# Kernel optimization log

Hardware: AMD Instinct MI355X
Metric: run time of the kernel (lower is better)

Reference implementation:

```python
import jax, jax.numpy as jnp
import numpy as np

# dims
B = 16        # batch
S = 32        # question seq len
H = 768       # bert-base hidden
E = 200000    # num entities
T = 200000    # padded triples per example
R = 500       # num relations
STEPS = 3     # num_steps
WAYS = 2      # num_ways


def setup_inputs() -> dict:
    key = jax.random.key(0)
    ks = jax.random.split(key, 10)
    # one-hot head entity per example (start distribution)
    head_ids = jax.random.randint(ks[0], (B,), 0, E)
    heads = jnp.zeros((B, E), jnp.float32).at[jnp.arange(B), head_ids].set(1.0)
    q_embeddings = jax.random.normal(ks[1], (B, H), jnp.float32)
    q_word_h = jax.random.normal(ks[2], (B, S, H), jnp.float32)
    attention_mask = jnp.ones((B, S), jnp.float32)
    # padded per-example triples (sub, rel, obj)
    sub = jax.random.randint(ks[3], (B, T), 0, E)
    rel = jax.random.randint(ks[4], (B, T), 0, R)
    obj = jax.random.randint(ks[5], (B, T), 0, E)
    triples = jnp.stack([sub, rel, obj], axis=-1).astype(jnp.int32)  # [B,T,3]
    scale = 0.02
    step_W = jax.random.normal(ks[6], (WAYS, STEPS, H, H), jnp.float32) * scale
    step_b = jnp.zeros((WAYS, STEPS, H), jnp.float32)
    rel_W = jax.random.normal(ks[7], (WAYS, H, R), jnp.float32) * scale
    rel_b = jnp.zeros((WAYS, R), jnp.float32)
    hop_W = jax.random.normal(ks[8], (WAYS, H, STEPS), jnp.float32) * scale
    hop_b = jnp.zeros((WAYS, STEPS), jnp.float32)
    return dict(heads=heads, q_embeddings=q_embeddings, q_word_h=q_word_h,
                attention_mask=attention_mask, step_W=step_W, step_b=step_b,
                rel_W=rel_W, rel_b=rel_b, hop_W=hop_W, hop_b=hop_b,
                triples=triples)


def _propagate(last_e, triples, rel_dist):
    # last_e: [E], triples: [T,3], rel_dist: [R] -> [E]
    sub, rel, obj = triples[:, 0], triples[:, 1], triples[:, 2]
    obj_p = last_e[sub] * rel_dist[rel]                 # gather + gate  [T]
    return jax.ops.segment_sum(obj_p, obj, num_segments=E)  # scatter-add [E]


def reference(heads, q_embeddings, q_word_h, attention_mask,
              step_W, step_b, rel_W, rel_b, hop_W, hop_b, triples):
    e_score = []
    for w in range(WAYS):
        last_e = heads                                   # [B,E]
        ent_probs = []
        for t in range(STEPS):
            cq_t = jnp.tanh(q_embeddings @ step_W[w, t] + step_b[w, t])   # [B,H]
            q_logits = jnp.einsum('bh,bsh->bs', cq_t, q_word_h)            # [B,S]
            q_dist = jax.nn.softmax(q_logits, axis=1) * attention_mask
            q_dist = q_dist / (jnp.sum(q_dist, axis=1, keepdims=True) + 1e-6)
            ctx_h = jnp.einsum('bs,bsh->bh', q_dist, q_word_h)             # [B,H]
            rel_dist = jax.nn.sigmoid(ctx_h @ rel_W[w] + rel_b[w])         # [B,R]
            last_e = jax.vmap(_propagate)(last_e, triples, rel_dist)      # [B,E]
            # renormalize entries > 1 (detached divisor, as in original)
            z = jax.lax.stop_gradient(jnp.where(last_e > 1.0, last_e, 1.0))
            last_e = last_e / z
            ent_probs.append(last_e)
        hop_res = jnp.stack(ent_probs, axis=1)                             # [B,STEPS,E]
        hop_attn = jax.nn.softmax(q_embeddings @ hop_W[w] + hop_b[w], axis=1)  # [B,STEPS]
        e_score.append(jnp.einsum('bse,bs->be', hop_res, hop_attn))
    return jnp.prod(jnp.stack(e_score), axis=0)                            # [B,E]
```

## Files before the change

kernel.cpp:

```cpp
#include <hip/hip_runtime.h>
#include <math.h>

#define NB 16
#define NS 32
#define NH 768
#define NE 200000
#define NT 200000
#define NR 500
#define NSTEPS 3
#define NWAYS 2

#define HSZ 2048
#define AHSZ 4096
#define BMW 6272
#define PCHUNK 40

typedef unsigned int u32;

__device__ __forceinline__ int fhash(int e) { return (int)(((u32)e * 2654435761u) >> 21); }
__device__ __forceinline__ int ahash(int e) { return (int)(((u32)e * 2654435761u) >> 20); }

__global__ __launch_bounds__(256) void cq_part_kernel(
    const float* __restrict__ qe, const float* __restrict__ stepW,
    float* __restrict__ part)
{
    int blk = blockIdx.x;
    int jc = blk % 12;
    int wt = (blk / 12) % 6;
    int kc = blk / 72;

    __shared__ float s_w[192][68];
    __shared__ float s_q[NB][196];

    int tid = threadIdx.x;
    int lane = tid & 63, wv = tid >> 6;

    {
        const float* Wbase = stepW + (size_t)wt * NH * NH + (size_t)(kc * 192) * NH + jc * 64;
#pragma unroll
        for (int u = 0; u < 12; ++u) {
            int f = tid + u * 256;
            int hh = f >> 4, c4 = (f & 15) * 4;
            float4 v = *(const float4*)(Wbase + (size_t)hh * NH + c4);
            *(float4*)&s_w[hh][c4] = v;
        }
    }
    {
#pragma unroll
        for (int u = 0; u < 3; ++u) {
            int f = tid + u * 256;
            int b = f / 48, c4 = (f % 48) * 4;
            float4 v = *(const float4*)(qe + (size_t)b * NH + kc * 192 + c4);
            *(float4*)&s_q[b][c4] = v;
        }
    }
    __syncthreads();

    float acc[4] = {0.f, 0.f, 0.f, 0.f};
#pragma unroll 4
    for (int h4 = 0; h4 < 48; ++h4) {
        float w0 = s_w[h4 * 4 + 0][lane];
        float w1 = s_w[h4 * 4 + 1][lane];
        float w2 = s_w[h4 * 4 + 2][lane];
        float w3 = s_w[h4 * 4 + 3][lane];
#pragma unroll
        for (int i = 0; i < 4; ++i) {
            float4 q = *(const float4*)&s_q[wv * 4 + i][h4 * 4];
            acc[i] += w0 * q.x + w1 * q.y + w2 * q.z + w3 * q.w;
        }
    }
#pragma unroll
    for (int i = 0; i < 4; ++i) {
        int b = wv * 4 + i;
        part[(((size_t)kc * 6 + wt) * NB + b) * NH + jc * 64 + lane] = acc[i];
    }
}

__global__ __launch_bounds__(256) void attn_kernel(
    const float* __restrict__ part, const float* __restrict__ stepB,
    const float* __restrict__ qwh, const float* __restrict__ mask,
    float* __restrict__ ctx)
{
    int b = blockIdx.x % NB;
    int wt = blockIdx.x / NB;

    __shared__ float s_cq[NH];
    __shared__ float s_sm[NS];

    int tid = threadIdx.x;

    for (int j = tid; j < NH; j += 256) {
        float a = stepB[wt * NH + j];
#pragma unroll
        for (int kc = 0; kc < 4; ++kc)
            a += part[(((size_t)kc * 6 + wt) * NB + b) * NH + j];
        s_cq[j] = tanhf(a);
    }
    __syncthreads();

    {
        int s = tid >> 3, l = tid & 7;
        const float* row = qwh + ((size_t)b * NS + s) * NH;
        float a = 0.f;
        for (int h = l; h < NH; h += 8) a += s_cq[h] * row[h];
        a += __shfl_down(a, 4, 8);
        a += __shfl_down(a, 2, 8);
        a += __shfl_down(a, 1, 8);
        if (l == 0) s_sm[s] = a;
    }
    __syncthreads();

    if (tid < 64) {
        float lg = (tid < 32) ? s_sm[tid] : -1e30f;
        float m = lg;
        for (int off = 16; off; off >>= 1) m = fmaxf(m, __shfl_xor(m, off, 32));
        float ev = expf(lg - m);
        float sum = ev;
        for (int off = 16; off; off >>= 1) sum += __shfl_xor(sum, off, 32);
        float d = ev / sum * ((tid < 32) ? mask[b * NS + tid] : 0.f);
        float sum2 = d;
        for (int off = 16; off; off >>= 1) sum2 += __shfl_xor(sum2, off, 32);
        d = d / (sum2 + 1e-6f);
        if (tid < 32) s_sm[tid] = d;
    }
    __syncthreads();

    for (int h = tid; h < NH; h += 256) {
        const float* col = qwh + (size_t)b * NS * NH + h;
        float c = 0.f;
#pragma unroll 8
        for (int s = 0; s < NS; ++s) c += s_sm[s] * col[s * NH];
        ctx[((size_t)wt * NB + b) * NH + h] = c;
    }
}

__global__ __launch_bounds__(256) void rel_part_kernel(
    const float* __restrict__ ctx, const float* __restrict__ relW,
    float* __restrict__ part_r)
{
    int blk = blockIdx.x;
    int rc = blk & 7;
    int w  = (blk >> 3) & 1;
    int kc = blk >> 4;

    __shared__ float s_ctx[48][68];

    int tid = threadIdx.x;
    int lane = tid & 63, wv = tid >> 6;

#pragma unroll
    for (int u = 0; u < 3; ++u) {
        int f = tid + u * 256;
        int tb = f >> 4, c4 = (f & 15) * 4;
        int t = tb >> 4, b = tb & 15;
        float4 v = *(const float4*)(ctx + ((size_t)(w * 3 + t) * NB + b) * NH + kc * 64 + c4);
        *(float4*)&s_ctx[tb][c4] = v;
    }
    __syncthreads();

    int col = rc * 64 + lane;
    int colc = col < NR ? col : NR - 1;
    const float* Wb = relW + (size_t)w * NH * NR + (size_t)(kc * 64) * NR + colc;

    float acc[12];
#pragma unroll
    for (int i = 0; i < 12; ++i) acc[i] = 0.f;

#pragma unroll 4
    for (int h4 = 0; h4 < 16; ++h4) {
        float w0 = Wb[(size_t)(h4 * 4 + 0) * NR];
        float w1 = Wb[(size_t)(h4 * 4 + 1) * NR];
        float w2 = Wb[(size_t)(h4 * 4 + 2) * NR];
        float w3 = Wb[(size_t)(h4 * 4 + 3) * NR];
#pragma unroll
        for (int i = 0; i < 12; ++i) {
            float4 c = *(const float4*)&s_ctx[wv * 12 + i][h4 * 4];
            acc[i] += w0 * c.x + w1 * c.y + w2 * c.z + w3 * c.w;
        }
    }
    if (col < NR) {
#pragma unroll
        for (int i = 0; i < 12; ++i) {
            int tb = wv * 12 + i;
            int t = tb >> 4, b = tb & 15;
            part_r[(((size_t)kc * 6 + (w * 3 + t)) * NB + b) * NR + col] = acc[i];
        }
    }
}

__global__ void rel_reduce_kernel(const float* __restrict__ part_r,
                                  const float* __restrict__ relB,
                                  float* __restrict__ rel)
{
    int b = blockIdx.x % NB;
    int wt = blockIdx.x / NB;
    int w = wt / NSTEPS;
    for (int r = threadIdx.x; r < NR; r += 256) {
        float a = relB[w * NR + r];
#pragma unroll
        for (int kc = 0; kc < 12; ++kc)
            a += part_r[(((size_t)kc * 6 + wt) * NB + b) * NR + r];
        rel[((size_t)wt * NB + b) * NR + r] = 1.f / (1.f + expf(-a));
    }
}

__global__ __launch_bounds__(192) void hop_kernel(
    const float* __restrict__ qe, const float* __restrict__ hopW,
    const float* __restrict__ hopB, float* __restrict__ hop)
{
    int wb = blockIdx.x;
    int w = wb / NB, b = wb % NB;
    int t = threadIdx.x / 64, l = threadIdx.x % 64;
    __shared__ float s_logit[4];
    float a = 0.f;
    for (int h = l; h < NH; h += 64) a += qe[b * NH + h] * hopW[((size_t)w * NH + h) * NSTEPS + t];
    for (int off = 32; off; off >>= 1) a += __shfl_down(a, off, 64);
    if (l == 0) s_logit[t] = a + hopB[w * NSTEPS + t];
    __syncthreads();
    if (threadIdx.x == 0) {
        float mx = fmaxf(s_logit[0], fmaxf(s_logit[1], s_logit[2]));
        float e0 = expf(s_logit[0] - mx), e1 = expf(s_logit[1] - mx), e2 = expf(s_logit[2] - mx);
        float inv = 1.f / (e0 + e1 + e2);
        hop[wb * NSTEPS + 0] = e0 * inv;
        hop[wb * NSTEPS + 1] = e1 * inv;
        hop[wb * NSTEPS + 2] = e2 * inv;
    }
}

__global__ void head_kernel(const float* __restrict__ heads, int* __restrict__ keys0,
                            float* __restrict__ vals0, u32* __restrict__ bm0)
{
    size_t N4 = (size_t)NB * NE / 4;
    const float4* h4 = (const float4*)heads;
    for (size_t i = (size_t)blockIdx.x * blockDim.x + threadIdx.x; i < N4;
         i += (size_t)gridDim.x * blockDim.x) {
        float4 v = h4[i];
        float c[4] = { v.x, v.y, v.z, v.w };
#pragma unroll
        for (int k = 0; k < 4; ++k) {
            if (c[k] != 0.0f) {
                size_t idx = i * 4 + k;
                int b = (int)(idx / NE);
                int e = (int)(idx % NE);
                int s = fhash(e);
                keys0[(size_t)b * HSZ + s] = e + 1;
                vals0[(size_t)b * HSZ + s] = 1.0f;
                vals0[(size_t)(NB + b) * HSZ + s] = 1.0f;
                atomicOr(&bm0[(size_t)b * BMW + (e >> 5)], 1u << (e & 31));
            }
        }
    }
}

__global__ __launch_bounds__(256) void prop_kernel(
    const int* __restrict__ triples,
    const u32* __restrict__ bmIn, const int* __restrict__ keysIn, const float* __restrict__ valsIn,
    u32* __restrict__ bmOut, int* __restrict__ keysOut, float* __restrict__ valsOut,
    const float* __restrict__ rel, int t)
{
    __shared__ u32 s_bm[BMW];
    int b = blockIdx.x / PCHUNK;
    int c = blockIdx.x % PCHUNK;
    const u32* g = bmIn + (size_t)b * BMW;
    for (int k = threadIdx.x; k < BMW; k += 256) s_bm[k] = g[k];
    __syncthreads();

    const int*   kin  = keysIn  + (size_t)b * HSZ;
    const float* v0in = valsIn  + (size_t)b * HSZ;
    const float* v1in = valsIn  + (size_t)(NB + b) * HSZ;
    const float* r0 = rel + ((size_t)(0 * NSTEPS + t) * NB + b) * NR;
    const float* r1 = rel + ((size_t)(1 * NSTEPS + t) * NB + b) * NR;
    int*   kout  = keysOut + (size_t)b * HSZ;
    float* v0out = valsOut + (size_t)b * HSZ;
    float* v1out = valsOut + (size_t)(NB + b) * HSZ;
    u32*   bmo   = bmOut + (size_t)b * BMW;

    const int4* tp = (const int4*)(triples + (size_t)b * NT * 3);
    const int QPC = (NT / 4) / PCHUNK;
    int qend = (c + 1) * QPC;
    for (int q = c * QPC + threadIdx.x; q < qend; q += 256) {
        int4 x = tp[q * 3 + 0];
        int4 y = tp[q * 3 + 1];
        int4 z = tp[q * 3 + 2];
        int su[4] = { x.x, x.w, y.z, z.y };
        int re[4] = { x.y, y.x, y.w, z.z };
        int ob[4] = { x.z, y.y, z.x, z.w };
#pragma unroll
        for (int k = 0; k < 4; ++k) {
            int sub = su[k];
            if ((s_bm[sub >> 5] >> (sub & 31)) & 1u) {
                int s = fhash(sub);
                float v0 = 0.f, v1 = 0.f;
                bool found = false;
                for (int p = 0; p < HSZ; ++p) {
                    int kk = kin[s];
                    if (kk == 0) break;
                    if (kk == sub + 1) {
                        v0 = fminf(v0in[s], 1.0f);
                        v1 = fminf(v1in[s], 1.0f);
                        found = true;
                        break;
                    }
                    s = (s + 1) & (HSZ - 1);
                }
                if (found) {
                    float c0 = v0 * r0[re[k]];
                    float c1 = v1 * r1[re[k]];
                    int e = ob[k];
                    int s2 = fhash(e);
                    for (int p = 0; p < HSZ; ++p) {
                        int old = atomicCAS(&kout[s2], 0, e + 1);
                        if (old == 0 || old == e + 1) {
                            atomicAdd(&v0out[s2], c0);
                            atomicAdd(&v1out[s2], c1);
                            if (old == 0) atomicOr(&bmo[e >> 5], 1u << (e & 31));
                            break;
                        }
                        s2 = (s2 + 1) & (HSZ - 1);
                    }
                }
            }
        }
    }
}

__global__ __launch_bounds__(256) void final_kernel(
    const int* __restrict__ keysG, const float* __restrict__ valsG,
    const float* __restrict__ hop, float* __restrict__ out)
{
    __shared__ int s_k[AHSZ];
    __shared__ float s_v0[AHSZ];
    __shared__ float s_v1[AHSZ];
    int b = blockIdx.x;
    for (int i = threadIdx.x; i < AHSZ; i += 256) { s_k[i] = 0; s_v0[i] = 0.f; s_v1[i] = 0.f; }
    __syncthreads();
    for (int gen = 1; gen <= 3; ++gen) {
        const int* kg = keysG + ((size_t)gen * NB + b) * HSZ;
        const float* vg = valsG + (size_t)gen * NWAYS * NB * HSZ;
        const float* v0 = vg + (size_t)b * HSZ;
        const float* v1 = vg + (size_t)(NB + b) * HSZ;
        float h0 = hop[(0 * NB + b) * NSTEPS + (gen - 1)];
        float h1 = hop[(1 * NB + b) * NSTEPS + (gen - 1)];
        for (int i = threadIdx.x; i < HSZ; i += 256) {
            int key = kg[i];
            if (key == 0) continue;
            float a0 = h0 * fminf(v0[i], 1.0f);
            float a1 = h1 * fminf(v1[i], 1.0f);
            int s = ahash(key - 1);
            for (int p = 0; p < AHSZ; ++p) {
                int old = atomicCAS(&s_k[s], 0, key);
                if (old == 0 || old == key) {
                    atomicAdd(&s_v0[s], a0);
                    atomicAdd(&s_v1[s], a1);
                    break;
                }
                s = (s + 1) & (AHSZ - 1);
            }
        }
    }
    __syncthreads();
    for (int i = threadIdx.x; i < AHSZ; i += 256) {
        int key = s_k[i];
        if (key) out[(size_t)b * NE + (key - 1)] = s_v0[i] * s_v1[i];
    }
}

extern "C" void kernel_launch(void* const* d_in, const int* in_sizes, int n_in,
                              void* d_out, int out_size, void* d_ws, size_t ws_size,
                              hipStream_t stream)
{
    const float* heads  = (const float*)d_in[0];
    const float* qe     = (const float*)d_in[1];
    const float* qwh    = (const float*)d_in[2];
    const float* mask   = (const float*)d_in[3];
    const float* stepW  = (const float*)d_in[4];
    const float* stepB  = (const float*)d_in[5];
    const float* relW   = (const float*)d_in[6];
    const float* relB   = (const float*)d_in[7];
    const float* hopW   = (const float*)d_in[8];
    const float* hopB   = (const float*)d_in[9];
    const int*   triples = (const int*)d_in[10];
    float* out = (float*)d_out;

    int*   keysG = (int*)d_ws;
    float* valsG = (float*)(keysG + 4 * NB * HSZ);
    u32*   bmG   = (u32*)(valsG + 4 * NWAYS * NB * HSZ);
    float* rel   = (float*)(bmG + 4 * (size_t)NB * BMW);
    float* hop   = rel + (size_t)NWAYS * NSTEPS * NB * NR;
    float* part  = hop + NWAYS * NB * NSTEPS;
    float* ctx   = part + (size_t)4 * 6 * NB * NH;
    float* part_r = ctx + (size_t)6 * NB * NH;

    size_t zero_bytes = (char*)rel - (char*)d_ws;
    hipMemsetAsync(d_ws, 0, zero_bytes, stream);
    hipMemsetAsync(d_out, 0, (size_t)NB * NE * sizeof(float), stream);

    cq_part_kernel<<<288, 256, 0, stream>>>(qe, stepW, part);
    hop_kernel<<<NWAYS * NB, 192, 0, stream>>>(qe, hopW, hopB, hop);
    head_kernel<<<2048, 256, 0, stream>>>(heads, keysG, valsG, bmG);
    attn_kernel<<<96, 256, 0, stream>>>(part, stepB, qwh, mask, ctx);
    rel_part_kernel<<<192, 256, 0, stream>>>(ctx, relW, part_r);
    rel_reduce_kernel<<<96, 256, 0, stream>>>(part_r, relB, rel);

    for (int t = 0; t < NSTEPS; ++t) {
        prop_kernel<<<NB * PCHUNK, 256, 0, stream>>>(
            triples,
            bmG + (size_t)t * NB * BMW,
            keysG + (size_t)t * NB * HSZ,
            valsG + (size_t)t * NWAYS * NB * HSZ,
            bmG + (size_t)(t + 1) * NB * BMW,
            keysG + (size_t)(t + 1) * NB * HSZ,
            valsG + (size_t)(t + 1) * NWAYS * NB * HSZ,
            rel, t);
    }

    final_kernel<<<NB, 256, 0, stream>>>(keysG, valsG, hop, out);
}
```

Measured before the change: 211.4 us.

## Fuse whole pipeline into one cooperative persistent kernel with grid syncs

Replaces the memsets and roughly ten separate kernel launches with a single cooperative kernel of 256 blocks. Phases are separated by grid.sync: zeroing, cq with fused tanh, head/hop, attention, the rel matmul, three propagation steps, and the final combine. The cq K-split reduction is folded into each block, and the rel sigmoid is computed on demand from partial sums. The aim is to remove launch overhead and inter-kernel gaps. The cost is fewer blocks for the propagation phase, redundant rel recomputation, and grid-wide barrier latency; a multi-launch fallback is kept in case the cooperative launch fails.

```diff
diff --git a/kernel.cpp b/kernel.cpp
--- a/kernel.cpp
+++ b/kernel.cpp
@@ -1,5 +1,8 @@
 #include <hip/hip_runtime.h>
+#include <hip/hip_cooperative_groups.h>
 #include <math.h>
+
+namespace cg = cooperative_groups;
 
 #define NB 16
 #define NS 32
@@ -13,355 +16,330 @@
 #define HSZ 2048
 #define AHSZ 4096
 #define BMW 6272
-#define PCHUNK 40
+#define GRID 256
+#define PCH 16
+#define QPB 50000
+#define QPC 3125
 
 typedef unsigned int u32;
 
 __device__ __forceinline__ int fhash(int e) { return (int)(((u32)e * 2654435761u) >> 21); }
 __device__ __forceinline__ int ahash(int e) { return (int)(((u32)e * 2654435761u) >> 20); }
 
-__global__ __launch_bounds__(256) void cq_part_kernel(
-    const float* __restrict__ qe, const float* __restrict__ stepW,
-    float* __restrict__ part)
+union SharedU {
+    struct { float w[192][68]; float q[NB][196]; } cq;
+    struct { u32 bm[BMW]; } pr;
+    struct { float ctx[48][68]; } rp;
+    struct { float cqv[NH]; float sm[NS]; } at;
+    struct { int k[AHSZ]; float v0[AHSZ]; float v1[AHSZ]; } fin;
+    struct { float logit[4]; } hp;
+};
+
+__device__ __forceinline__ float rel_val(const float* __restrict__ part_r,
+                                         const float* __restrict__ relB,
+                                         int w, int t, int b, int r)
 {
+    int wt = w * NSTEPS + t;
+    float a = relB[w * NR + r];
+#pragma unroll
+    for (int kc = 0; kc < 12; ++kc)
+        a += part_r[(((size_t)kc * 6 + wt) * NB + b) * NR + r];
+    return 1.f / (1.f + expf(-a));
+}
+
+__global__ __launch_bounds__(256) void fused_kernel(
+    const float* __restrict__ heads, const float* __restrict__ qe,
+    const float* __restrict__ qwh,  const float* __restrict__ mask,
+    const float* __restrict__ stepW, const float* __restrict__ stepB,
+    const float* __restrict__ relW, const float* __restrict__ relB,
+    const float* __restrict__ hopW, const float* __restrict__ hopB,
+    const int* __restrict__ triples, float* __restrict__ out,
+    int* keysG, float* valsG, u32* bmG, float* hop,
+    float* cqf, float* ctx, float* part_r, int phase)
+{
+    cg::grid_group grid = cg::this_grid();
+    __shared__ SharedU S;
+    int tid = threadIdx.x;
     int blk = blockIdx.x;
-    int jc = blk % 12;
-    int wt = (blk / 12) % 6;
-    int kc = blk / 72;
-
-    __shared__ float s_w[192][68];
-    __shared__ float s_q[NB][196];
-
-    int tid = threadIdx.x;
     int lane = tid & 63, wv = tid >> 6;
-
-    {
-        const float* Wbase = stepW + (size_t)wt * NH * NH + (size_t)(kc * 192) * NH + jc * 64;
-#pragma unroll
-        for (int u = 0; u < 12; ++u) {
-            int f = tid + u * 256;
-            int hh = f >> 4, c4 = (f & 15) * 4;
-            float4 v = *(const float4*)(Wbase + (size_t)hh * NH + c4);
-            *(float4*)&s_w[hh][c4] = v;
-        }
-    }
-    {
+    bool all = (phase < 0);
+
+    if (all || phase == 0) {
+        const int ZW4 = (4 * NB * HSZ + 4 * NWAYS * NB * HSZ + 4 * NB * BMW) / 4;
+        float4 z = make_float4(0.f, 0.f, 0.f, 0.f);
+        float4* z1 = (float4*)keysG;
+        for (int i = blk * 256 + tid; i < ZW4; i += gridDim.x * 256) z1[i] = z;
+        float4* z2 = (float4*)out;
+        const int OW4 = NB * NE / 4;
+        for (int i = blk * 256 + tid; i < OW4; i += gridDim.x * 256) z2[i] = z;
+    }
+    if (all) grid.sync();
+
+    if (all || phase == 1) {
+        if (blk < 72) {
+            int wt = blk / 12, jc = blk % 12;
+            float acc[4] = {0.f, 0.f, 0.f, 0.f};
+            for (int kc = 0; kc < 4; ++kc) {
+                if (kc) __syncthreads();
+                const float* Wbase = stepW + (size_t)wt * NH * NH + (size_t)(kc * 192) * NH + jc * 64;
+#pragma unroll
+                for (int u = 0; u < 12; ++u) {
+                    int f = tid + u * 256;
+                    int hh = f >> 4, c4 = (f & 15) * 4;
+                    *(float4*)&S.cq.w[hh][c4] = *(const float4*)(Wbase + (size_t)hh * NH + c4);
+                }
+#pragma unroll
+                for (int u = 0; u < 3; ++u) {
+                    int f = tid + u * 256;
+                    int b = f / 48, c4 = (f % 48) * 4;
+                    *(float4*)&S.cq.q[b][c4] = *(const float4*)(qe + (size_t)b * NH + kc * 192 + c4);
+                }
+                __syncthreads();
+#pragma unroll 4
+                for (int h4 = 0; h4 < 48; ++h4) {
+                    float w0 = S.cq.w[h4 * 4 + 0][lane];
+                    float w1 = S.cq.w[h4 * 4 + 1][lane];
+                    float w2 = S.cq.w[h4 * 4 + 2][lane];
+                    float w3 = S.cq.w[h4 * 4 + 3][lane];
+#pragma unroll
+                    for (int i = 0; i < 4; ++i) {
+                        float4 q = *(const float4*)&S.cq.q[wv * 4 + i][h4 * 4];
+                        acc[i] += w0 * q.x + w1 * q.y + w2 * q.z + w3 * q.w;
+                    }
+                }
+            }
+            int j = jc * 64 + lane;
+#pragma unroll
+            for (int i = 0; i < 4; ++i) {
+                int b = wv * 4 + i;
+                cqf[((size_t)wt * NB + b) * NH + j] = tanhf(acc[i] + stepB[wt * NH + j]);
+            }
+        } else if (blk < 224) {
+            const float4* h4 = (const float4*)heads;
+            for (int i = (blk - 72) * 256 + tid; i < NB * NE / 4; i += 152 * 256) {
+                float4 v = h4[i];
+                float c[4] = { v.x, v.y, v.z, v.w };
+#pragma unroll
+                for (int k = 0; k < 4; ++k) {
+                    if (c[k] != 0.0f) {
+                        int idx = i * 4 + k;
+                        int b = idx / NE, e = idx % NE;
+                        int s = fhash(e);
+                        keysG[(size_t)b * HSZ + s] = e + 1;
+                        valsG[(size_t)b * HSZ + s] = 1.0f;
+                        valsG[(size_t)(NB + b) * HSZ + s] = 1.0f;
+                        atomicOr(&bmG[(size_t)b * BMW + (e >> 5)], 1u << (e & 31));
+                    }
+                }
+            }
+        } else {
+            int wb = blk - 224;
+            int w = wb / NB, b = wb % NB;
+            if (wv < 3) {
+                float a = 0.f;
+                for (int h = lane; h < NH; h += 64)
+                    a += qe[b * NH + h] * hopW[((size_t)w * NH + h) * NSTEPS + wv];
+                for (int off = 32; off; off >>= 1) a += __shfl_down(a, off, 64);
+                if (lane == 0) S.hp.logit[wv] = a + hopB[w * NSTEPS + wv];
+            }
+            __syncthreads();
+            if (tid == 0) {
+                float mx = fmaxf(S.hp.logit[0], fmaxf(S.hp.logit[1], S.hp.logit[2]));
+                float e0 = expf(S.hp.logit[0] - mx), e1 = expf(S.hp.logit[1] - mx), e2 = expf(S.hp.logit[2] - mx);
+                float inv = 1.f / (e0 + e1 + e2);
+                hop[wb * NSTEPS + 0] = e0 * inv;
+                hop[wb * NSTEPS + 1] = e1 * inv;
+                hop[wb * NSTEPS + 2] = e2 * inv;
+            }
+        }
+    }
+    if (all) grid.sync();
+
+    if ((all || phase == 2) && blk < 96) {
+        int b = blk % NB, wt = blk / NB;
+        for (int j = tid; j < NH; j += 256)
+            S.at.cqv[j] = cqf[((size_t)wt * NB + b) * NH + j];
+        __syncthreads();
+        {
+            int s = tid >> 3, l = tid & 7;
+            const float* row = qwh + ((size_t)b * NS + s) * NH;
+            float a = 0.f;
+            for (int h = l; h < NH; h += 8) a += S.at.cqv[h] * row[h];
+            a += __shfl_down(a, 4, 8);
+            a += __shfl_down(a, 2, 8);
+            a += __shfl_down(a, 1, 8);
+            if (l == 0) S.at.sm[s] = a;
+        }
+        __syncthreads();
+        if (tid < 64) {
+            float lg = (tid < 32) ? S.at.sm[tid] : -1e30f;
+            float m = lg;
+            for (int off = 16; off; off >>= 1) m = fmaxf(m, __shfl_xor(m, off, 32));
+            float ev = expf(lg - m);
+            float sum = ev;
+            for (int off = 16; off; off >>= 1) sum += __shfl_xor(sum, off, 32);
+            float d = ev / sum * ((tid < 32) ? mask[b * NS + tid] : 0.f);
+            float sum2 = d;
+            for (int off = 16; off; off >>= 1) sum2 += __shfl_xor(sum2, off, 32);
+            d = d / (sum2 + 1e-6f);
+            if (tid < 32) S.at.sm[tid] = d;
+        }
+        __syncthreads();
+        for (int h = tid; h < NH; h += 256) {
+            const float* col = qwh + (size_t)b * NS * NH + h;
+            float c = 0.f;
+#pragma unroll 8
+            for (int s = 0; s < NS; ++s) c += S.at.sm[s] * col[s * NH];
+            ctx[((size_t)wt * NB + b) * NH + h] = c;
+        }
+    }
+    if (all) grid.sync();
+
+    if ((all || phase == 3) && blk < 192) {
+        int rc = blk & 7, w = (blk >> 3) & 1, kc = blk >> 4;
 #pragma unroll
         for (int u = 0; u < 3; ++u) {
             int f = tid + u * 256;
-            int b = f / 48, c4 = (f % 48) * 4;
-            float4 v = *(const float4*)(qe + (size_t)b * NH + kc * 192 + c4);
-            *(float4*)&s_q[b][c4] = v;
-        }
-    }
-    __syncthreads();
-
-    float acc[4] = {0.f, 0.f, 0.f, 0.f};
+            int tb = f >> 4, c4 = (f & 15) * 4;
+            int t = tb >> 4, b = tb & 15;
+            *(float4*)&S.rp.ctx[tb][c4] =
+                *(const float4*)(ctx + ((size_t)(w * 3 + t) * NB + b) * NH + kc * 64 + c4);
+        }
+        __syncthreads();
+        int col = rc * 64 + lane;
+        int colc = col < NR ? col : NR - 1;
+        const float* Wb = relW + (size_t)w * NH * NR + (size_t)(kc * 64) * NR + colc;
+        float acc[12];
+#pragma unroll
+        for (int i = 0; i < 12; ++i) acc[i] = 0.f;
 #pragma unroll 4
-    for (int h4 = 0; h4 < 48; ++h4) {
-        float w0 = s_w[h4 * 4 + 0][lane];
-        float w1 = s_w[h4 * 4 + 1][lane];
-        float w2 = s_w[h4 * 4 + 2][lane];
-        float w3 = s_w[h4 * 4 + 3][lane];
-#pragma unroll
-        for (int i = 0; i < 4; ++i) {
-            float4 q = *(const float4*)&s_q[wv * 4 + i][h4 * 4];
-            acc[i] += w0 * q.x + w1 * q.y + w2 * q.z + w3 * q.w;
-        }
-    }
-#pragma unroll
-    for (int i = 0; i < 4; ++i) {
-        int b = wv * 4 + i;
-        part[(((size_t)kc * 6 + wt) * NB + b) * NH + jc * 64 + lane] = acc[i];
-    }
-}
-
-__global__ __launch_bounds__(256) void attn_kernel(
-    const float* __restrict__ part, const float* __restrict__ stepB,
-    const float* __restrict__ qwh, const float* __restrict__ mask,
-    float* __restrict__ ctx)
-{
-    int b = blockIdx.x % NB;
-    int wt = blockIdx.x / NB;
-
-    __shared__ float s_cq[NH];
-    __shared__ float s_sm[NS];
-
-    int tid = threadIdx.x;
-
-    for (int j = tid; j < NH; j += 256) {
-        float a = stepB[wt * NH + j];
-#pragma unroll
-        for (int kc = 0; kc < 4; ++kc)
-            a += part[(((size_t)kc * 6 + wt) * NB + b) * NH + j];
-        s_cq[j] = tanhf(a);
-    }
-    __syncthreads();
-
-    {
-        int s = tid >> 3, l = tid & 7;
-        const float* row = qwh + ((size_t)b * NS + s) * NH;
-        float a = 0.f;
-        for (int h = l; h < NH; h += 8) a += s_cq[h] * row[h];
-        a += __shfl_down(a, 4, 8);
-        a += __shfl_down(a, 2, 8);
-        a += __shfl_down(a, 1, 8);
-        if (l == 0) s_sm[s] = a;
-    }
-    __syncthreads();
-
-    if (tid < 64) {
-        float lg = (tid < 32) ? s_sm[tid] : -1e30f;
-        float m = lg;
-        for (int off = 16; off; off >>= 1) m = fmaxf(m, __shfl_xor(m, off, 32));
-        float ev = expf(lg - m);
-        float sum = ev;
-        for (int off = 16; off; off >>= 1) sum += __shfl_xor(sum, off, 32);
-        float d = ev / sum * ((tid < 32) ? mask[b * NS + tid] : 0.f);
-        float sum2 = d;
-        for (int off = 16; off; off >>= 1) sum2 += __shfl_xor(sum2, off, 32);
-        d = d / (sum2 + 1e-6f);
-        if (tid < 32) s_sm[tid] = d;
-    }
-    __syncthreads();
-
-    for (int h = tid; h < NH; h += 256) {
-        const float* col = qwh + (size_t)b * NS * NH + h;
-        float c = 0.f;
-#pragma unroll 8
-        for (int s = 0; s < NS; ++s) c += s_sm[s] * col[s * NH];
-        ctx[((size_t)wt * NB + b) * NH + h] = c;
-    }
-}
-
-__global__ __launch_bounds__(256) void rel_part_kernel(
-    const float* __restrict__ ctx, const float* __restrict__ relW,
-    float* __restrict__ part_r)
-{
-    int blk = blockIdx.x;
-    int rc = blk & 7;
-    int w  = (blk >> 3) & 1;
-    int kc = blk >> 4;
-
-    __shared__ float s_ctx[48][68];
-
-    int tid = threadIdx.x;
-    int lane = tid & 63, wv = tid >> 6;
-
-#pragma unroll
-    for (int u = 0; u < 3; ++u) {
-        int f = tid + u * 256;
-        int tb = f >> 4, c4 = (f & 15) * 4;
-        int t = tb >> 4, b = tb & 15;
-        float4 v = *(const float4*)(ctx + ((size_t)(w * 3 + t) * NB + b) * NH + kc * 64 + c4);
-        *(float4*)&s_ctx[tb][c4] = v;
-    }
-    __syncthreads();
-
-    int col = rc * 64 + lane;
-    int colc = col < NR ? col : NR - 1;
-    const float* Wb = relW + (size_t)w * NH * NR + (size_t)(kc * 64) * NR + colc;
-
-    float acc[12];
-#pragma unroll
-    for (int i = 0; i < 12; ++i) acc[i] = 0.f;
-
-#pragma unroll 4
-    for (int h4 = 0; h4 < 16; ++h4) {
-        float w0 = Wb[(size_t)(h4 * 4 + 0) * NR];
-        float w1 = Wb[(size_t)(h4 * 4 + 1) * NR];
-        float w2 = Wb[(size_t)(h4 * 4 + 2) * NR];
-        float w3 = Wb[(size_t)(h4 * 4 + 3) * NR];
-#pragma unroll
-        for (int i = 0; i < 12; ++i) {
-            float4 c = *(const float4*)&s_ctx[wv * 12 + i][h4 * 4];
-            acc[i] += w0 * c.x + w1 * c.y + w2 * c.z + w3 * c.w;
-        }
-    }
-    if (col < NR) {
-#pragma unroll
-        for (int i = 0; i < 12; ++i) {
-            int tb = wv * 12 + i;
-            int t = tb >> 4, b = tb & 15;
-            part_r[(((size_t)kc * 6 + (w * 3 + t)) * NB + b) * NR + col] = acc[i];
-        }
-    }
-}
-
-__global__ void rel_reduce_kernel(const float* __restrict__ part_r,
-                                  const float* __restrict__ relB,
-                                  float* __restrict__ rel)
-{
-    int b = blockIdx.x % NB;
-    int wt = blockIdx.x / NB;
-    int w = wt / NSTEPS;
-    for (int r = threadIdx.x; r < NR; r += 256) {
-        float a = relB[w * NR + r];
-#pragma unroll
-        for (int kc = 0; kc < 12; ++kc)
-            a += part_r[(((size_t)kc * 6 + wt) * NB + b) * NR + r];
-        rel[((size_t)wt * NB + b) * NR + r] = 1.f / (1.f + expf(-a));
-    }
-}
-
-__global__ __launch_bounds__(192) void hop_kernel(
-    const float* __restrict__ qe, const float* __restrict__ hopW,
-    const float* __restrict__ hopB, float* __restrict__ hop)
-{
-    int wb = blockIdx.x;
-    int w = wb / NB, b = wb % NB;
-    int t = threadIdx.x / 64, l = threadIdx.x % 64;
-    __shared__ float s_logit[4];
-    float a = 0.f;
-    for (int h = l; h < NH; h += 64) a += qe[b * NH + h] * hopW[((size_t)w * NH + h) * NSTEPS + t];
-    for (int off = 32; off; off >>= 1) a += __shfl_down(a, off, 64);
-    if (l == 0) s_logit[t] = a + hopB[w * NSTEPS + t];
-    __syncthreads();
-    if (threadIdx.x == 0) {
-        float mx = fmaxf(s_logit[0], fmaxf(s_logit[1], s_logit[2]));
-        float e0 = expf(s_logit[0] - mx), e1 = expf(s_logit[1] - mx), e2 = expf(s_logit[2] - mx);
-        float inv = 1.f / (e0 + e1 + e2);
-        hop[wb * NSTEPS + 0] = e0 * inv;
-        hop[wb * NSTEPS + 1] = e1 * inv;
-        hop[wb * NSTEPS + 2] = e2 * inv;
-    }
-}
-
-__global__ void head_kernel(const float* __restrict__ heads, int* __restrict__ keys0,
-                            float* __restrict__ vals0, u32* __restrict__ bm0)
-{
-    size_t N4 = (size_t)NB * NE / 4;
-    const float4* h4 = (const float4*)heads;
-    for (size_t i = (size_t)blockIdx.x * blockDim.x + threadIdx.x; i < N4;
-         i += (size_t)gridDim.x * blockDim.x) {
-        float4 v = h4[i];
-        float c[4] = { v.x, v.y, v.z, v.w };
-#pragma unroll
-        for (int k = 0; k < 4; ++k) {
-            if (c[k] != 0.0f) {
-                size_t idx = i * 4 + k;
-                int b = (int)(idx / NE);
-                int e = (int)(idx % NE);
-                int s = fhash(e);
-                keys0[(size_t)b * HSZ + s] = e + 1;
-                vals0[(size_t)b * HSZ + s] = 1.0f;
-                vals0[(size_t)(NB + b) * HSZ + s] = 1.0f;
-                atomicOr(&bm0[(size_t)b * BMW + (e >> 5)], 1u << (e & 31));
-            }
-        }
-    }
-}
-
-__global__ __launch_bounds__(256) void prop_kernel(
-    const int* __restrict__ triples,
-    const u32* __restrict__ bmIn, const int* __restrict__ keysIn, const float* __restrict__ valsIn,
-    u32* __restrict__ bmOut, int* __restrict__ keysOut, float* __restrict__ valsOut,
-    const float* __restrict__ rel, int t)
-{
-    __shared__ u32 s_bm[BMW];
-    int b = blockIdx.x / PCHUNK;
-    int c = blockIdx.x % PCHUNK;
-    const u32* g = bmIn + (size_t)b * BMW;
-    for (int k = threadIdx.x; k < BMW; k += 256) s_bm[k] = g[k];
-    __syncthreads();
-
-    const int*   kin  = keysIn  + (size_t)b * HSZ;
-    const float* v0in = valsIn  + (size_t)b * HSZ;
-    const float* v1in = valsIn  + (size_t)(NB + b) * HSZ;
-    const float* r0 = rel + ((size_t)(0 * NSTEPS + t) * NB + b) * NR;
-    const float* r1 = rel + ((size_t)(1 * NSTEPS + t) * NB + b) * NR;
-    int*   kout  = keysOut + (size_t)b * HSZ;
-    float* v0out = valsOut + (size_t)b * HSZ;
-    float* v1out = valsOut + (size_t)(NB + b) * HSZ;
-    u32*   bmo   = bmOut + (size_t)b * BMW;
-
-    const int4* tp = (const int4*)(triples + (size_t)b * NT * 3);
-    const int QPC = (NT / 4) / PCHUNK;
-    int qend = (c + 1) * QPC;
-    for (int q = c * QPC + threadIdx.x; q < qend; q += 256) {
-        int4 x = tp[q * 3 + 0];
-        int4 y = tp[q * 3 + 1];
-        int4 z = tp[q * 3 + 2];
-        int su[4] = { x.x, x.w, y.z, z.y };
-        int re[4] = { x.y, y.x, y.w, z.z };
-        int ob[4] = { x.z, y.y, z.x, z.w };
-#pragma unroll
-        for (int k = 0; k < 4; ++k) {
-            int sub = su[k];
-            if ((s_bm[sub >> 5] >> (sub & 31)) & 1u) {
-                int s = fhash(sub);
-                float v0 = 0.f, v1 = 0.f;
-                bool found = false;
-                for (int p = 0; p < HSZ; ++p) {
-                    int kk = kin[s];
-                    if (kk == 0) break;
-                    if (kk == sub + 1) {
-                        v0 = fminf(v0in[s], 1.0f);
-                        v1 = fminf(v1in[s], 1.0f);
-                        found = true;
+        for (int h4 = 0; h4 < 16; ++h4) {
+            float w0 = Wb[(size_t)(h4 * 4 + 0) * NR];
+            float w1 = Wb[(size_t)(h4 * 4 + 1) * NR];
+            float w2 = Wb[(size_t)(h4 * 4 + 2) * NR];
+            float w3 = Wb[(size_t)(h4 * 4 + 3) * NR];
+#pragma unroll
+            for (int i = 0; i < 12; ++i) {
+                float4 c = *(const float4*)&S.rp.ctx[wv * 12 + i][h4 * 4];
+                acc[i] += w0 * c.x + w1 * c.y + w2 * c.z + w3 * c.w;
+            }
+        }
+        if (col < NR) {
+#pragma unroll
+            for (int i = 0; i < 12; ++i) {
+                int tb = wv * 12 + i;
+                int t = tb >> 4, b = tb & 15;
+                part_r[(((size_t)kc * 6 + (w * 3 + t)) * NB + b) * NR + col] = acc[i];
+            }
+        }
+    }
+    if (all) grid.sync();
+
+    for (int t = 0; t < NSTEPS; ++t) {
+        if (all || phase == 4 + t) {
+            int b = blk / PCH, c = blk % PCH;
+            const u32* bmIn   = bmG + (size_t)t * NB * BMW;
+            const int* keysIn = keysG + (size_t)t * NB * HSZ;
+            const float* valsIn = valsG + (size_t)t * NWAYS * NB * HSZ;
+            u32* bmOut   = bmG + (size_t)(t + 1) * NB * BMW;
+            int* keysOut = keysG + (size_t)(t + 1) * NB * HSZ;
+            float* valsOut = valsG + (size_t)(t + 1) * NWAYS * NB * HSZ;
+
+            const u32* g = bmIn + (size_t)b * BMW;
+            for (int k = tid; k < BMW; k += 256) S.pr.bm[k] = g[k];
+            __syncthreads();
+
+            const int*   kin  = keysIn + (size_t)b * HSZ;
+            const float* v0in = valsIn + (size_t)b * HSZ;
+            const float* v1in = valsIn + (size_t)(NB + b) * HSZ;
+            int*   kout  = keysOut + (size_t)b * HSZ;
+            float* v0out = valsOut + (size_t)b * HSZ;
+            float* v1out = valsOut + (size_t)(NB + b) * HSZ;
+            u32*   bmo   = bmOut + (size_t)b * BMW;
+
+            const int4* tp = (const int4*)(triples + (size_t)b * NT * 3);
+            int qend = (c + 1) * QPC;
+            for (int q = c * QPC + tid; q < qend; q += 256) {
+                int4 x = tp[q * 3 + 0];
+                int4 y = tp[q * 3 + 1];
+                int4 z = tp[q * 3 + 2];
+                int su[4] = { x.x, x.w, y.z, z.y };
+                int re[4] = { x.y, y.x, y.w, z.z };
+                int ob[4] = { x.z, y.y, z.x, z.w };
+#pragma unroll
+                for (int k = 0; k < 4; ++k) {
+                    int sub = su[k];
+                    if ((S.pr.bm[sub >> 5] >> (sub & 31)) & 1u) {
+                        int s = fhash(sub);
+                        float v0 = 0.f, v1 = 0.f;
+                        bool found = false;
+                        for (int p = 0; p < HSZ; ++p) {
+                            int kk = kin[s];
+                            if (kk == 0) break;
+                            if (kk == sub + 1) {
+                                v0 = fminf(v0in[s], 1.0f);
+                                v1 = fminf(v1in[s], 1.0f);
+                                found = true;
+                                break;
+                            }
+                            s = (s + 1) & (HSZ - 1);
+                        }
+                        if (found) {
+                            float c0 = v0 * rel_val(part_r, relB, 0, t, b, re[k]);
+                            float c1 = v1 * rel_val(part_r, relB, 1, t, b, re[k]);
+                            int e = ob[k];
+                            int s2 = fhash(e);
+                            for (int p = 0; p < HSZ; ++p) {
+                                int old = atomicCAS(&kout[s2], 0, e + 1);
+                                if (old == 0 || old == e + 1) {
+                                    atomicAdd(&v0out[s2], c0);
+                                    atomicAdd(&v1out[s2], c1);
+                                    if (old == 0) atomicOr(&bmo[e >> 5], 1u << (e & 31));
+                                    break;
+                                }
+                                s2 = (s2 + 1) & (HSZ - 1);
+                            }
+                        }
+                    }
+                }
+            }
+        }
+        if (all) grid.sync();
+    }
+
+    if ((all || phase == 7) && blk < NB) {
+        int b = blk;
+        for (int i = tid; i < AHSZ; i += 256) { S.fin.k[i] = 0; S.fin.v0[i] = 0.f; S.fin.v1[i] = 0.f; }
+        __syncthreads();
+        for (int gen = 1; gen <= 3; ++gen) {
+            const int* kg = keysG + ((size_t)gen * NB + b) * HSZ;
+            const float* vg = valsG + (size_t)gen * NWAYS * NB * HSZ;
+            const float* v0 = vg + (size_t)b * HSZ;
+            const float* v1 = vg + (size_t)(NB + b) * HSZ;
+            float h0 = hop[(0 * NB + b) * NSTEPS + (gen - 1)];
+            float h1 = hop[(1 * NB + b) * NSTEPS + (gen - 1)];
+            for (int i = tid; i < HSZ; i += 256) {
+                int key = kg[i];
+                if (key == 0) continue;
+                float a0 = h0 * fminf(v0[i], 1.0f);
+                float a1 = h1 * fminf(v1[i], 1.0f);
+                int s = ahash(key - 1);
+                for (int p = 0; p < AHSZ; ++p) {
+                    int old = atomicCAS(&S.fin.k[s], 0, key);
+                    if (old == 0 || old == key) {
+                        atomicAdd(&S.fin.v0[s], a0);
+                        atomicAdd(&S.fin.v1[s], a1);
                         break;
                     }
-                    s = (s + 1) & (HSZ - 1);
-                }
-                if (found) {
-                    float c0 = v0 * r0[re[k]];
-                    float c1 = v1 * r1[re[k]];
-                    int e = ob[k];
-                    int s2 = fhash(e);
-                    for (int p = 0; p < HSZ; ++p) {
-                        int old = atomicCAS(&kout[s2], 0, e + 1);
-                        if (old == 0 || old == e + 1) {
-                            atomicAdd(&v0out[s2], c0);
-                            atomicAdd(&v1out[s2], c1);
-                            if (old == 0) atomicOr(&bmo[e >> 5], 1u << (e & 31));
-                            break;
-                        }
-                        s2 = (s2 + 1) & (HSZ - 1);
-                    }
-                }
-            }
-        }
-    }
-}
-
-__global__ __launch_bounds__(256) void final_kernel(
-    const int* __restrict__ keysG, const float* __restrict__ valsG,
-    const float* __restrict__ hop, float* __restrict__ out)
-{
-    __shared__ int s_k[AHSZ];
-    __shared__ float s_v0[AHSZ];
-    __shared__ float s_v1[AHSZ];
-    int b = blockIdx.x;
-    for (int i = threadIdx.x; i < AHSZ; i += 256) { s_k[i] = 0; s_v0[i] = 0.f; s_v1[i] = 0.f; }
-    __syncthreads();
-    for (int gen = 1; gen <= 3; ++gen) {
-        const int* kg = keysG + ((size_t)gen * NB + b) * HSZ;
-        const float* vg = valsG + (size_t)gen * NWAYS * NB * HSZ;
-        const float* v0 = vg + (size_t)b * HSZ;
-        const float* v1 = vg + (size_t)(NB + b) * HSZ;
-        float h0 = hop[(0 * NB + b) * NSTEPS + (gen - 1)];
-        float h1 = hop[(1 * NB + b) * NSTEPS + (gen - 1)];
-        for (int i = threadIdx.x; i < HSZ; i += 256) {
-            int key = kg[i];
-            if (key == 0) continue;
-            float a0 = h0 * fminf(v0[i], 1.0f);
-            float a1 = h1 * fminf(v1[i], 1.0f);
-            int s = ahash(key - 1);
-            for (int p = 0; p < AHSZ; ++p) {
-                int old = atomicCAS(&s_k[s], 0, key);
-                if (old == 0 || old == key) {
-                    atomicAdd(&s_v0[s], a0);
-                    atomicAdd(&s_v1[s], a1);
-                    break;
-                }
-                s = (s + 1) & (AHSZ - 1);
-            }
-        }
-    }
-    __syncthreads();
-    for (int i = threadIdx.x; i < AHSZ; i += 256) {
-        int key = s_k[i];
-        if (key) out[(size_t)b * NE + (key - 1)] = s_v0[i] * s_v1[i];
+                    s = (s + 1) & (AHSZ - 1);
+                }
+            }
+        }
+        __syncthreads();
+        for (int i = tid; i < AHSZ; i += 256) {
+            int key = S.fin.k[i];
+            if (key) out[(size_t)b * NE + (key - 1)] = S.fin.v0[i] * S.fin.v1[i];
+        }
     }
 }
 
@@ -385,34 +363,41 @@
     int*   keysG = (int*)d_ws;
     float* valsG = (float*)(keysG + 4 * NB * HSZ);
     u32*   bmG   = (u32*)(valsG + 4 * NWAYS * NB * HSZ);
-    float* rel   = (float*)(bmG + 4 * (size_t)NB * BMW);
-    float* hop   = rel + (size_t)NWAYS * NSTEPS * NB * NR;
-    float* part  = hop + NWAYS * NB * NSTEPS;
-    float* ctx   = part + (size_t)4 * 6 * NB * NH;
+    float* hop   = (float*)(bmG + 4 * (size_t)NB * BMW);
+    float* cqf   = hop + NWAYS * NB * NSTEPS;
+    float* ctx   = cqf + (size_t)6 * NB * NH;
     float* part_r = ctx + (size_t)6 * NB * NH;
 
-    size_t zero_bytes = (char*)rel - (char*)d_ws;
-    hipMemsetAsync(d_ws, 0, zero_bytes, stream);
-    hipMemsetAsync(d_out, 0, (size_t)NB * NE * sizeof(float), stream);
-
-    cq_part_kernel<<<288, 256, 0, stream>>>(qe, stepW, part);
-    hop_kernel<<<NWAYS * NB, 192, 0, stream>>>(qe, hopW, hopB, hop);
-    head_kernel<<<2048, 256, 0, stream>>>(heads, keysG, valsG, bmG);
-    attn_kernel<<<96, 256, 0, stream>>>(part, stepB, qwh, mask, ctx);
-    rel_part_kernel<<<192, 256, 0, stream>>>(ctx, relW, part_r);
-    rel_reduce_kernel<<<96, 256, 0, stream>>>(part_r, relB, rel);
-
-    for (int t = 0; t < NSTEPS; ++t) {
-        prop_kernel<<<NB * PCHUNK, 256, 0, stream>>>(
-            triples,
-            bmG + (size_t)t * NB * BMW,
-            keysG + (size_t)t * NB * HSZ,
-            valsG + (size_t)t * NWAYS * NB * HSZ,
-            bmG + (size_t)(t + 1) * NB * BMW,
-            keysG + (size_t)(t + 1) * NB * HSZ,
-            valsG + (size_t)(t + 1) * NWAYS * NB * HSZ,
-            rel, t);
-    }
-
-    final_kernel<<<NB, 256, 0, stream>>>(keysG, valsG, hop, out);
+    int phase = -1;
+    void* args[] = {
+        (void*)&heads, (void*)&qe, (void*)&qwh, (void*)&mask,
+        (void*)&stepW, (void*)&stepB, (void*)&relW, (void*)&relB,
+        (void*)&hopW, (void*)&hopB, (void*)&triples, (void*)&out,
+        (void*)&keysG, (void*)&valsG, (void*)&bmG, (void*)&hop,
+        (void*)&cqf, (void*)&ctx, (void*)&part_r, (void*)&phase
+    };
+    hipError_t err = hipLaunchCooperativeKernel((void*)fused_kernel, dim3(GRID), dim3(256),
+                                                args, 0, stream);
+    if (err != hipSuccess) {
+        (void)hipGetLastError();
+        fused_kernel<<<256, 256, 0, stream>>>(heads, qe, qwh, mask, stepW, stepB, relW, relB,
+                                              hopW, hopB, triples, out, keysG, valsG, bmG, hop,
+                                              cqf, ctx, part_r, 0);
+        fused_kernel<<<256, 256, 0, stream>>>(heads, qe, qwh, mask, stepW, stepB, relW, relB,
+                                              hopW, hopB, triples, out, keysG, valsG, bmG, hop,
+                                              cqf, ctx, part_r, 1);
+        fused_kernel<<<96, 256, 0, stream>>>(heads, qe, qwh, mask, stepW, stepB, relW, relB,
+                                             hopW, hopB, triples, out, keysG, valsG, bmG, hop,
+                                             cqf, ctx, part_r, 2);
+        fused_kernel<<<192, 256, 0, stream>>>(heads, qe, qwh, mask, stepW, stepB, relW, relB,
+                                              hopW, hopB, triples, out, keysG, valsG, bmG, hop,
+                                              cqf, ctx, part_r, 3);
+        for (int t = 0; t < NSTEPS; ++t)
+            fused_kernel<<<256, 256, 0, stream>>>(heads, qe, qwh, mask, stepW, stepB, relW, relB,
+                                                  hopW, hopB, triples, out, keysG, valsG, bmG, hop,
+                                                  cqf, ctx, part_r, 4 + t);
+        fused_kernel<<<16, 256, 0, stream>>>(heads, qe, qwh, mask, stepW, stepB, relW, relB,
+                                             hopW, hopB, triples, out, keysG, valsG, bmG, hop,
+                                             cqf, ctx, part_r, 7);
+    }
 }
```

Result: slower. 423.8 us (+100.5%).
